# Kernel optimization log

Hardware: AMD Instinct MI355X
Metric: run time of the kernel (lower is better)

Reference implementation:

```python
import jax, jax.numpy as jnp
import numpy as np

N = 50000      # nodes
E = 800000     # edges (avg degree 16)
C_IN = 128
C_HID = 256
C_OUT = 256
SLOPE = 0.2    # LeakyReLU negative slope (PyG GATv2Conv default)


def gatv2_layer(x, src, dst, edge_attr, Wl, Wr, We, att, bias):
    """PyG GATv2Conv, heads=1, share_weights=False.
    e_ij = att . leaky_relu(Wl x_j + Wr x_i + We e_ij); softmax over incoming
    edges of each target i; out_i = sum_j alpha_ij * (Wl x_j) + bias."""
    xl = x @ Wl                       # [N, out] source transform
    xr = x @ Wr                       # [N, out] target transform
    ee = edge_attr[:, None] @ We      # [E, out] edge feature transform (edge_dim=1)
    m = xl[src] + xr[dst] + ee        # [E, out] per-edge message pre-activation
    e = jnp.einsum('ed,d->e', jax.nn.leaky_relu(m, SLOPE), att)  # [E]
    # segment softmax over target nodes
    emax = jax.ops.segment_max(e, dst, num_segments=N)           # [N]
    ex = jnp.exp(e - emax[dst])                                  # [E]
    denom = jax.ops.segment_sum(ex, dst, num_segments=N)         # [N]
    alpha = ex / denom[dst]                                      # [E]
    out = jax.ops.segment_sum(xl[src] * alpha[:, None], dst, num_segments=N)
    return out + bias


def setup_inputs() -> dict:
    key = jax.random.key(0)
    ks = jax.random.split(key, 24)

    def lin(k, i, o):
        return (jax.random.normal(k, (i, o), jnp.float32) / np.sqrt(i)).astype(jnp.float32)

    inp = {
        'features': jax.random.normal(ks[0], (N, C_IN), jnp.float32),
        'edge_index': jax.random.randint(ks[1], (2, E), 0, N, dtype=jnp.int64),
        'edge_attr': jax.random.uniform(ks[2], (E,), jnp.float32),
        # conv1: c_in -> c_hidden
        'Wl1': lin(ks[3], C_IN, C_HID), 'Wr1': lin(ks[4], C_IN, C_HID),
        'We1': lin(ks[5], 1, C_HID),
        'a1': jax.random.normal(ks[6], (C_HID,), jnp.float32) / np.sqrt(C_HID),
        'bb1': jnp.zeros((C_HID,), jnp.float32),
        # conv2: c_hidden -> c_hidden
        'Wl2': lin(ks[7], C_HID, C_HID), 'Wr2': lin(ks[8], C_HID, C_HID),
        'We2': lin(ks[9], 1, C_HID),
        'a2': jax.random.normal(ks[10], (C_HID,), jnp.float32) / np.sqrt(C_HID),
        'bb2': jnp.zeros((C_HID,), jnp.float32),
        # conv3: c_hidden -> c_out (concat=False, heads=1 -> same math)
        'Wl3': lin(ks[11], C_HID, C_OUT), 'Wr3': lin(ks[12], C_HID, C_OUT),
        'We3': lin(ks[13], 1, C_OUT),
        'a3': jax.random.normal(ks[14], (C_OUT,), jnp.float32) / np.sqrt(C_OUT),
        'bb3': jnp.zeros((C_OUT,), jnp.float32),
        # MLP head: Linear(c_out,10) -> relu -> Linear(10,1); dropout is eval-mode identity
        'Wh1': lin(ks[15], C_OUT, 10), 'bh1': jnp.zeros((10,), jnp.float32),
        'Wh2': lin(ks[16], 10, 1), 'bh2': jnp.zeros((1,), jnp.float32),
    }
    return inp


def reference(features, edge_index, edge_attr,
              Wl1, Wr1, We1, a1, bb1,
              Wl2, Wr2, We2, a2, bb2,
              Wl3, Wr3, We3, a3, bb3,
              Wh1, bh1, Wh2, bh2):
    src, dst = edge_index[0], edge_index[1]
    x1 = jax.nn.relu(gatv2_layer(features, src, dst, edge_attr, Wl1, Wr1, We1, a1, bb1))
    x2 = jax.nn.relu(gatv2_layer(x1, src, dst, edge_attr, Wl2, Wr2, We2, a2, bb2))
    x3 = jax.nn.relu(gatv2_layer(x2, src, dst, edge_attr, Wl3, Wr3, We3, a3, bb3))
    x4 = jnp.max(x3, axis=-2)                 # global max pool over nodes -> [c_out]
    x5 = jax.nn.relu(x4 @ Wh1 + bh1)          # [10]
    return x5 @ Wh2 + bh2                     # [1]
```

## Files before the change

### kernel.cpp

```cpp
#include <hip/hip_runtime.h>
#include <cstddef>
#include <cstdint>

typedef __attribute__((ext_vector_type(8))) short short8v;
typedef __attribute__((ext_vector_type(4))) short short4v;
typedef __attribute__((ext_vector_type(4))) float floatx4;

__device__ __forceinline__ float b2f(short u){
    return __uint_as_float(((unsigned)(unsigned short)u) << 16);
}
__device__ __forceinline__ short f2b(float f){
    unsigned x = __float_as_uint(f);
    unsigned r = x + 0x7FFFu + ((x >> 16) & 1u);
    return (short)(r >> 16);
}
__device__ __forceinline__ float loadF(const void* p, size_t i, int isBf16){
    return isBf16 ? b2f(((const short*)p)[i]) : ((const float*)p)[i];
}
__device__ __forceinline__ int loadI(const void* p, size_t i, int isI64){
    return isI64 ? ((const int*)p)[2 * i] : ((const int*)p)[i];
}
__device__ __forceinline__ void gload16(const void* g, void* l){
    __builtin_amdgcn_global_load_lds(
        (const __attribute__((address_space(1))) void*)g,
        (__attribute__((address_space(3))) void*)l, 16, 0, 0);
}

__global__ void setup_kernel(const void* feat, const void* ei, int N, int* flags,
                             int* cnt, int* fill, unsigned* pool, void* out){
    int gid = blockIdx.x * 256 + threadIdx.x;
    if (gid < N){ cnt[gid] = 0; fill[gid] = 0; }
    if (gid < 256) pool[gid] = 0u;
    if (blockIdx.x == 0){
        int t = threadIdx.x;
        if (t < 64){
            if (t >= 8 && t < 16) flags[t] = 0;
            const unsigned short* fs = (const unsigned short*)feat;
            int plaus = 0;
            for (int j = t; j < 128; j += 64){
                unsigned short s = fs[2 * j];
                int e = (s >> 7) & 0xFF;
                if (s == 0 || (e >= 100 && e <= 140)) plaus++;
            }
            #pragma unroll
            for (int o = 32; o > 0; o >>= 1) plaus += __shfl_xor(plaus, o);
            const int* ew = (const int*)ei;
            int zeros = 0;
            for (int j = t; j < 128; j += 64) if (ew[2 * j + 1] == 0) zeros++;
            #pragma unroll
            for (int o = 32; o > 0; o >>= 1) zeros += __shfl_xor(zeros, o);
            if (t == 0){
                flags[0] = (plaus >= 64) ? 1 : 0;
                flags[1] = (zeros >= 64) ? 1 : 0;
            }
        }
        __syncthreads();
        if (threadIdx.x == 0){
            if (flags[0]) ((short*)out)[0] = f2b(777.0f);
            else          ((float*)out)[0] = 777.0f;
        }
    }
}

__global__ void sentinel_kernel(void* out, const int* flags, float v){
    if (threadIdx.x == 0){
        if (flags[0]) ((short*)out)[0] = f2b(v);
        else          ((float*)out)[0] = v;
    }
}

__global__ void hist_kernel(const void* __restrict__ ei, int* __restrict__ cnt, int E,
                            const int* __restrict__ flags){
    int i = blockIdx.x * 256 + threadIdx.x;
    if (i < E) atomicAdd(&cnt[loadI(ei, (size_t)E + i, flags[1])], 1);
}

__global__ void scanA(const int* __restrict__ cnt, int* __restrict__ off,
                      int* __restrict__ partial, int N){
    __shared__ int wsum[16];
    const int t = threadIdx.x, w = t >> 6, lane = t & 63;
    int i = blockIdx.x * 1024 + t;
    int v = (i < N) ? cnt[i] : 0;
    int x = v;
    #pragma unroll
    for (int o = 1; o < 64; o <<= 1){
        int y = __shfl_up(x, o);
        if (lane >= o) x += y;
    }
    if (lane == 63) wsum[w] = x;
    __syncthreads();
    if (w == 0){
        int mv = (lane < 16) ? wsum[lane] : 0;
        int xx = mv;
        #pragma unroll
        for (int o = 1; o < 16; o <<= 1){
            int y = __shfl_up(xx, o);
            if (lane >= o) xx += y;
        }
        if (lane < 16) wsum[lane] = xx - mv;
    }
    __syncthreads();
    int incl = x + wsum[w];
    if (i < N) off[i] = incl - v;
    if (t == 1023) partial[blockIdx.x] = incl;
}

__global__ void scanB(int* __restrict__ partial, int* __restrict__ off, int nb, int N){
    int lane = threadIdx.x;
    int v = (lane < nb) ? partial[lane] : 0;
    int x = v;
    #pragma unroll
    for (int o = 1; o < 64; o <<= 1){
        int y = __shfl_up(x, o);
        if (lane >= o) x += y;
    }
    if (lane < nb) partial[lane] = x - v;
    if (lane == 63) off[N] = x;
}

__global__ void scanC(int* __restrict__ off, const int* __restrict__ partial, int N){
    int i = blockIdx.x * 1024 + threadIdx.x;
    if (i < N) off[i] += partial[blockIdx.x];
}

__global__ void scatter_kernel(const void* __restrict__ ei, const void* __restrict__ ea,
                               const int* __restrict__ off, int* __restrict__ fill,
                               int* __restrict__ srcS, float* __restrict__ eaS,
                               int E, const int* __restrict__ flags){
    int i = blockIdx.x * 256 + threadIdx.x;
    if (i >= E) return;
    int d = loadI(ei, (size_t)E + i, flags[1]);
    int pos = off[d] + atomicAdd(&fill[d], 1);
    srcS[pos] = loadI(ei, (size_t)i, flags[1]);
    eaS[pos] = loadF(ea, (size_t)i, flags[0]);
}

struct PJobs { const void* W[6]; short* bhi[6]; short* blo[6]; int K[6]; int fidx[6]; };
__global__ void prep_all(PJobs J, int* __restrict__ flags){
    int j = blockIdx.y;
    int K = J.K[j];
    if (blockIdx.x >= K) return;
    int idx = blockIdx.x * 256 + threadIdx.x;
    int k = idx >> 8, c = idx & 255;
    float v = loadF(J.W[j], idx, flags[0]);
    short h = f2b(v);
    short l = f2b(v - b2f(h));
    J.bhi[j][(size_t)c * K + k] = h;
    J.blo[j][(size_t)c * K + k] = l;
    if (__ballot(l != 0) != 0ull && (threadIdx.x & 63) == 0) atomicOr(&flags[J.fidx[j]], 1);
}

struct DJob { const void* src; float* dst; int n; };
struct DJobs { DJob j[13]; };
__global__ void decode_many(DJobs jobs, const int* __restrict__ flags){
    const DJob J = jobs.j[blockIdx.x];
    int fbf = flags[0];
    for (int i = threadIdx.x; i < J.n; i += 256)
        J.dst[i] = loadF(J.src, (size_t)i, fbf);
}

template<int BZ>
__global__ __launch_bounds__(512, 2) void gemm_tpl(
        const void* __restrict__ A, const short* __restrict__ Alo, int aRaw,
        const short* __restrict__ Bhi, const short* __restrict__ Blo,
        float* __restrict__ C, int M, int K,
        const int* __restrict__ flags, const int* __restrict__ bLoFlag){
    if (BZ ? (bLoFlag[0] != 0) : (bLoFlag[0] == 0)) return;
    __shared__ __align__(16) short Ah[2][256 * 32];
    __shared__ __align__(16) short Al[2][256 * 32];
    __shared__ __align__(16) short Bh[2][64 * 32];
    __shared__ __align__(16) short Bl[2][BZ ? 8 : 64 * 32];
    const int fbf = flags[0];
    const int az   = (aRaw && fbf) ? 1 : 0;
    const int aF32 = (aRaw && !fbf) ? 1 : 0;
    const int t = threadIdx.x;
    const int w = t >> 6, lane = t & 63;
    const int wrow = w >> 1, wcol = w & 1;
    const int bRow = blockIdx.x * 256;
    const int bCol = blockIdx.y * 64;
    const short* Ahp = (const short*)A;
    const float* Af  = (const float*)A;

    floatx4 acc[4][2];
    #pragma unroll
    for (int m = 0; m < 4; m++)
        #pragma unroll
        for (int n = 0; n < 2; n++) acc[m][n] = (floatx4){0.f, 0.f, 0.f, 0.f};

    auto STAGE = [&](int buf, int kk){
        if (!aF32){
            #pragma unroll
            for (int iss = 0; iss < 2; iss++){
                int ci  = (iss * 8 + w) * 64 + lane;
                int row = ci >> 2;
                int cg  = (ci & 3) ^ (row & 3);
                int gr = bRow + row; if (gr >= M) gr = M - 1;
                size_t ga = (size_t)gr * K + kk + cg * 8;
                int seg = (iss * 8 + w) * 512;
                gload16(&Ahp[ga], &Ah[buf][seg]);
                if (!az) gload16(&Alo[ga], &Al[buf][seg]);
            }
        } else {
            #pragma unroll
            for (int i2 = 0; i2 < 2; i2++){
                int e = i2 * 512 + t;
                int row = e >> 2, cl = e & 3;
                int slot = cl ^ (row & 3);
                int gr = bRow + row; if (gr >= M) gr = M - 1;
                size_t ga = (size_t)gr * K + kk + cl * 8;
                floatx4 v0 = *(const floatx4*)&Af[ga];
                floatx4 v1 = *(const floatx4*)&Af[ga + 4];
                short8v h, l;
                #pragma unroll
                for (int j = 0; j < 4; j++){
                    short hj = f2b(v0[j]);
                    h[j] = hj; l[j] = f2b(v0[j] - b2f(hj));
                    short hk = f2b(v1[j]);
                    h[4 + j] = hk; l[4 + j] = f2b(v1[j] - b2f(hk));
                }
                *(short8v*)&Ah[buf][row * 32 + slot * 8] = h;
                *(short8v*)&Al[buf][row * 32 + slot * 8] = l;
            }
        }
        {
            int ci  = w * 32 + (lane & 31);
            int row = ci >> 2;
            int cg  = (ci & 3) ^ (row & 3);
            size_t gb = (size_t)(bCol + row) * K + kk + cg * 8;
            int seg = w * 256;
            if (lane < 32){
                gload16(&Bhi[gb], &Bh[buf][seg]);
                if (!BZ) gload16(&Blo[gb], &Bl[buf][seg]);
            }
        }
    };

    const int T = K >> 5;
    STAGE(0, 0);
    int cur = 0;
    for (int kt = 0; kt < T; ++kt){
        if (kt + 1 < T) STAGE(cur ^ 1, (kt + 1) << 5);
        if (aF32){
            asm volatile("s_waitcnt vmcnt(0) lgkmcnt(0)" ::: "memory");
        } else if (kt + 1 >= T){
            asm volatile("s_waitcnt vmcnt(0)" ::: "memory");
        } else if (az){
            if (BZ) asm volatile("s_waitcnt vmcnt(3)" ::: "memory");
            else    asm volatile("s_waitcnt vmcnt(4)" ::: "memory");
        } else {
            if (BZ) asm volatile("s_waitcnt vmcnt(5)" ::: "memory");
            else    asm volatile("s_waitcnt vmcnt(6)" ::: "memory");
        }
        __builtin_amdgcn_s_barrier();
        const int g = lane >> 4;
        short8v a_h[4], a_l[4], b_h[2], b_l[2];
        #pragma unroll
        for (int m = 0; m < 4; m++){
            int ar = wrow * 64 + m * 16 + (lane & 15);
            int co = ((g ^ (ar & 3)) << 3);
            a_h[m] = *(const short8v*)&Ah[cur][ar * 32 + co];
            if (!az) a_l[m] = *(const short8v*)&Al[cur][ar * 32 + co];
        }
        #pragma unroll
        for (int n = 0; n < 2; n++){
            int br = wcol * 32 + n * 16 + (lane & 15);
            int co = ((g ^ (br & 3)) << 3);
            b_h[n] = *(const short8v*)&Bh[cur][br * 32 + co];
            if (!BZ) b_l[n] = *(const short8v*)&Bl[cur][br * 32 + co];
        }
        #pragma unroll
        for (int m = 0; m < 4; m++)
            #pragma unroll
            for (int n = 0; n < 2; n++){
                if (!az) acc[m][n] = __builtin_amdgcn_mfma_f32_16x16x32_bf16(
                                         a_l[m], b_h[n], acc[m][n], 0, 0, 0);
                if (!BZ) acc[m][n] = __builtin_amdgcn_mfma_f32_16x16x32_bf16(
                                         a_h[m], b_l[n], acc[m][n], 0, 0, 0);
                acc[m][n] = __builtin_amdgcn_mfma_f32_16x16x32_bf16(
                                a_h[m], b_h[n], acc[m][n], 0, 0, 0);
            }
        __builtin_amdgcn_s_barrier();
        cur ^= 1;
    }
    #pragma unroll
    for (int m = 0; m < 4; m++){
        int rb = bRow + wrow * 64 + m * 16 + ((lane >> 4) << 2);
        #pragma unroll
        for (int n = 0; n < 2; n++){
            int cg = bCol + wcol * 32 + n * 16 + (lane & 15);
            #pragma unroll
            for (int r = 0; r < 4; r++){
                int gr = rb + r;
                if (gr < M) C[(size_t)gr * 512 + cg] = acc[m][n][r];
            }
        }
    }
}

__global__ __launch_bounds__(256) void fused_agg(const float* __restrict__ PR,
        const int* __restrict__ srcS, const float* __restrict__ eaS,
        const int* __restrict__ off, const float* __restrict__ WeF,
        const float* __restrict__ attF, const float* __restrict__ bbF,
        short* __restrict__ QHi, short* __restrict__ QLo, int N){
    int node = blockIdx.x * 4 + (threadIdx.x >> 6);
    int lane = threadIdx.x & 63;
    if (node >= N) return;
    const int beg = off[node], end = off[node + 1];
    const int dd = lane << 2;
    const floatx4 xr4 = *(const floatx4*)&PR[(size_t)node * 512 + 256 + dd];
    const floatx4 we4 = *(const floatx4*)&WeF[dd];
    const floatx4 at4 = *(const floatx4*)&attF[dd];
    float m = -1e30f, ssum = 0.f;
    floatx4 a4 = (floatx4){0.f, 0.f, 0.f, 0.f};
    for (int k0 = beg; k0 < end; k0 += 8){
        floatx4 v[8]; float pp[8]; float eav[8];
        #pragma unroll
        for (int c = 0; c < 8; c++){
            int k = k0 + c; if (k >= end) k = end - 1;
            int s = srcS[k];
            eav[c] = eaS[k];
            v[c] = *(const floatx4*)&PR[(size_t)s * 512 + dd];
        }
        #pragma unroll
        for (int c = 0; c < 8; c++){
            float p = 0.f;
            #pragma unroll
            for (int j = 0; j < 4; j++){
                float tv = v[c][j] + xr4[j] + eav[c] * we4[j];
                tv = tv > 0.f ? tv : 0.2f * tv;
                p += tv * at4[j];
            }
            #pragma unroll
            for (int o = 32; o > 0; o >>= 1) p += __shfl_xor(p, o);
            pp[c] = (k0 + c < end) ? p : -1e30f;
        }
        float pm = pp[0];
        #pragma unroll
        for (int c = 1; c < 8; c++) pm = fmaxf(pm, pp[c]);
        float newm = fmaxf(m, pm);
        float scale = __expf(m - newm);
        ssum *= scale;
        a4[0] *= scale; a4[1] *= scale; a4[2] *= scale; a4[3] *= scale;
        #pragma unroll
        for (int c = 0; c < 8; c++){
            float wgt = __expf(pp[c] - newm);
            ssum += wgt;
            a4[0] += wgt * v[c][0]; a4[1] += wgt * v[c][1];
            a4[2] += wgt * v[c][2]; a4[3] += wgt * v[c][3];
        }
        m = newm;
    }
    float inv = (end > beg) ? 1.f / ssum : 0.f;
    short4v h4, l4;
    #pragma unroll
    for (int j = 0; j < 4; j++){
        float o = fmaxf(a4[j] * inv + bbF[dd + j], 0.f);
        short h = f2b(o);
        h4[j] = h;
        l4[j] = f2b(o - b2f(h));
    }
    *(short4v*)&QHi[(size_t)node * 256 + dd] = h4;
    *(short4v*)&QLo[(size_t)node * 256 + dd] = l4;
}

__global__ __launch_bounds__(256) void col_max2(const short* __restrict__ hi,
        const short* __restrict__ lo, unsigned* __restrict__ pool, int N){
    int lane = threadIdx.x & 63;
    int w = threadIdx.x >> 6;
    int dd = lane << 2;
    floatx4 mx = (floatx4){0.f, 0.f, 0.f, 0.f};
    for (int r = blockIdx.x * 4 + w; r < N; r += gridDim.x * 4){
        short4v h = *(const short4v*)&hi[(size_t)r * 256 + dd];
        short4v l = *(const short4v*)&lo[(size_t)r * 256 + dd];
        mx[0] = fmaxf(mx[0], b2f(h[0]) + b2f(l[0]));
        mx[1] = fmaxf(mx[1], b2f(h[1]) + b2f(l[1]));
        mx[2] = fmaxf(mx[2], b2f(h[2]) + b2f(l[2]));
        mx[3] = fmaxf(mx[3], b2f(h[3]) + b2f(l[3]));
    }
    atomicMax(&pool[dd + 0], __float_as_uint(mx[0]));
    atomicMax(&pool[dd + 1], __float_as_uint(mx[1]));
    atomicMax(&pool[dd + 2], __float_as_uint(mx[2]));
    atomicMax(&pool[dd + 3], __float_as_uint(mx[3]));
}

__global__ void head_kernel(const unsigned* __restrict__ pool, const float* __restrict__ Wh1F,
        const float* __restrict__ bh1F, const float* __restrict__ Wh2F,
        const float* __restrict__ bh2F, void* __restrict__ out, const int* __restrict__ flags){
    int lane = threadIdx.x;
    float acc = 0.f;
    if (lane < 10){
        acc = bh1F[lane];
        for (int d = 0; d < 256; ++d)
            acc += __uint_as_float(pool[d]) * Wh1F[d * 10 + lane];
        acc = fmaxf(acc, 0.f) * Wh2F[lane];
    }
    #pragma unroll
    for (int o = 32; o > 0; o >>= 1) acc += __shfl_xor(acc, o);
    if (lane == 0){
        float r = acc + bh2F[0];
        if (flags[0]) ((short*)out)[0] = f2b(r);
        else          ((float*)out)[0] = r;
    }
}

extern "C" void kernel_launch(void* const* d_in, const int* in_sizes, int n_in,
                              void* d_out, int out_size, void* d_ws, size_t ws_size,
                              hipStream_t stream){
    const void* feat = d_in[0];
    const void* ei   = d_in[1];
    const void* ea   = d_in[2];
    const void* Wl[3] = {d_in[3], d_in[8],  d_in[13]};
    const void* Wr[3] = {d_in[4], d_in[9],  d_in[14]};
    const void* We[3] = {d_in[5], d_in[10], d_in[15]};
    const void* at[3] = {d_in[6], d_in[11], d_in[16]};
    const void* bb[3] = {d_in[7], d_in[12], d_in[17]};
    const void* Wh1 = d_in[18];
    const void* bh1 = d_in[19];
    const void* Wh2 = d_in[20];
    const void* bh2 = d_in[21];

    const int N = in_sizes[0] / 128;
    const int E = in_sizes[1] / 2;
    const int Kin[3] = {128, 256, 256};
    const int nb = (N + 1023) / 1024;

    char* p = (char*)d_ws;
    auto alloc = [&](size_t bytes) -> void* {
        void* r = (void*)p; p += (bytes + 255) & ~(size_t)255; return r;
    };
    int*   flags   = (int*)alloc(256);
    int*   partial = (int*)alloc(256 * 4);
    int*   off   = (int*)alloc((size_t)(N + 1) * 4);
    int*   cnt   = (int*)alloc((size_t)N * 4);
    int*   fill  = (int*)alloc((size_t)N * 4);
    int*   srcS  = (int*)alloc((size_t)E * 4);
    float* eaS   = (float*)alloc((size_t)E * 4);
    float* PR    = (float*)alloc((size_t)N * 512 * 4);
    short* QHi   = (short*)alloc((size_t)N * 256 * 2);
    short* QLo   = (short*)alloc((size_t)N * 256 * 2);
    short* BtH[3]; short* BtL[3];
    for (int i = 0; i < 3; i++){
        BtH[i] = (short*)alloc((size_t)512 * Kin[i] * 2);
        BtL[i] = (short*)alloc((size_t)512 * Kin[i] * 2);
    }
    float* WeF  = (float*)alloc(3 * 256 * 4);
    float* attF = (float*)alloc(3 * 256 * 4);
    float* bbF  = (float*)alloc(3 * 256 * 4);
    float* Wh1F = (float*)alloc(2560 * 4);
    float* bh1F = (float*)alloc(16 * 4);
    float* Wh2F = (float*)alloc(16 * 4);
    float* bh2F = (float*)alloc(4 * 4);
    unsigned* pool = (unsigned*)alloc(256 * 4);
    size_t need = (size_t)(p - (char*)d_ws);

    setup_kernel<<<dim3((N + 255) / 256), dim3(256), 0, stream>>>(feat, ei, N, flags,
                                                                  cnt, fill, pool, d_out);
    if (need > ws_size){
        sentinel_kernel<<<dim3(1), dim3(1), 0, stream>>>(d_out, flags, 555.0f);
        return;
    }

    hist_kernel<<<dim3((E + 255) / 256), dim3(256), 0, stream>>>(ei, cnt, E, flags);
    scanA<<<dim3(nb), dim3(1024), 0, stream>>>(cnt, off, partial, N);
    scanB<<<dim3(1), dim3(64), 0, stream>>>(partial, off, nb, N);
    scanC<<<dim3(nb), dim3(1024), 0, stream>>>(off, partial, N);
    scatter_kernel<<<dim3((E + 255) / 256), dim3(256), 0, stream>>>(ei, ea, off, fill,
                                                                    srcS, eaS, E, flags);
    PJobs pj;
    for (int i = 0; i < 3; i++){
        pj.W[2 * i]     = Wl[i];
        pj.bhi[2 * i]   = BtH[i];
        pj.blo[2 * i]   = BtL[i];
        pj.W[2 * i + 1]   = Wr[i];
        pj.bhi[2 * i + 1] = BtH[i] + (size_t)256 * Kin[i];
        pj.blo[2 * i + 1] = BtL[i] + (size_t)256 * Kin[i];
        pj.K[2 * i] = pj.K[2 * i + 1] = Kin[i];
        pj.fidx[2 * i] = pj.fidx[2 * i + 1] = 8 + i;
    }
    prep_all<<<dim3(256, 6), dim3(256), 0, stream>>>(pj, flags);

    DJobs jobs;
    for (int i = 0; i < 3; i++){
        jobs.j[i]     = { We[i], WeF  + i * 256, 256 };
        jobs.j[3 + i] = { at[i], attF + i * 256, 256 };
        jobs.j[6 + i] = { bb[i], bbF  + i * 256, 256 };
    }
    jobs.j[9]  = { Wh1, Wh1F, 2560 };
    jobs.j[10] = { bh1, bh1F, 10 };
    jobs.j[11] = { Wh2, Wh2F, 10 };
    jobs.j[12] = { bh2, bh2F, 1 };
    decode_many<<<dim3(13), dim3(256), 0, stream>>>(jobs, flags);

    dim3 gemm_grid((N + 255) / 256, 8);
    for (int L = 0; L < 3; L++){
        const void* A = (L == 0) ? feat : (const void*)QHi;
        int aRaw = (L == 0) ? 1 : 0;
        gemm_tpl<1><<<gemm_grid, dim3(512), 0, stream>>>(A, QLo, aRaw, BtH[L], BtL[L],
                                                         PR, N, Kin[L], flags, &flags[8 + L]);
        gemm_tpl<0><<<gemm_grid, dim3(512), 0, stream>>>(A, QLo, aRaw, BtH[L], BtL[L],
                                                         PR, N, Kin[L], flags, &flags[8 + L]);
        fused_agg<<<dim3((N + 3) / 4), dim3(256), 0, stream>>>(PR, srcS, eaS, off,
                                                               WeF + L * 256, attF + L * 256,
                                                               bbF + L * 256, QHi, QLo, N);
    }
    col_max2<<<dim3(256), dim3(256), 0, stream>>>(QHi, QLo, pool, N);
    head_kernel<<<dim3(1), dim3(64), 0, stream>>>(pool, Wh1F, bh1F, Wh2F, bh2F, d_out, flags);
    (void)n_in; (void)out_size;
}
```

Before: 892.4 us.

## Retile GEMM to 128x128 blocks, specialize A-zero path, use DPP wave reduction

The split-bf16 GEMM moves from 256x64 tiles with 512 threads to 128x128 tiles with 256 threads, each wave now computing a 64x64 sub-tile, and B staging is merged into the same load loop. A new template variant skips the A-low products and their loads entirely when the raw input is already bf16. This aims for better operand reuse per tile and higher occupancy. The aggregation kernel's shuffle-xor reduction is replaced by a DPP row-shift reduction with a final readlane, and it gets an occupancy hint. The trade-off is more accumulator registers per thread and more kernel launches in the first layer.

```diff
diff --git a/kernel.cpp b/kernel.cpp
--- a/kernel.cpp
+++ b/kernel.cpp
@@ -24,6 +24,21 @@
     __builtin_amdgcn_global_load_lds(
         (const __attribute__((address_space(1))) void*)g,
         (__attribute__((address_space(3))) void*)l, 16, 0, 0);
+}
+
+template<int CTRL, int RM>
+__device__ __forceinline__ float dppAdd(float p){
+    int t = __builtin_amdgcn_update_dpp(0, __float_as_int(p), CTRL, RM, 0xF, true);
+    return p + __int_as_float(t);
+}
+__device__ __forceinline__ float waveSum(float p){
+    p = dppAdd<0xB1, 0xF>(p);
+    p = dppAdd<0x4E, 0xF>(p);
+    p = dppAdd<0x141, 0xF>(p);
+    p = dppAdd<0x140, 0xF>(p);
+    p = dppAdd<0x142, 0xA>(p);
+    p = dppAdd<0x143, 0xC>(p);
+    return __int_as_float(__builtin_amdgcn_readlane(__float_as_int(p), 63));
 }
 
 __global__ void setup_kernel(const void* feat, const void* ei, int N, int* flags,
@@ -159,52 +174,60 @@
         J.dst[i] = loadF(J.src, (size_t)i, fbf);
 }
 
-template<int BZ>
-__global__ __launch_bounds__(512, 2) void gemm_tpl(
+template<int AZT, int BZ>
+__global__ __launch_bounds__(256, (AZT && BZ) ? 4 : 3) void gemm_tpl(
         const void* __restrict__ A, const short* __restrict__ Alo, int aRaw,
         const short* __restrict__ Bhi, const short* __restrict__ Blo,
         float* __restrict__ C, int M, int K,
         const int* __restrict__ flags, const int* __restrict__ bLoFlag){
-    if (BZ ? (bLoFlag[0] != 0) : (bLoFlag[0] == 0)) return;
-    __shared__ __align__(16) short Ah[2][256 * 32];
-    __shared__ __align__(16) short Al[2][256 * 32];
-    __shared__ __align__(16) short Bh[2][64 * 32];
-    __shared__ __align__(16) short Bl[2][BZ ? 8 : 64 * 32];
     const int fbf = flags[0];
-    const int az   = (aRaw && fbf) ? 1 : 0;
-    const int aF32 = (aRaw && !fbf) ? 1 : 0;
+    const int azr = (aRaw && fbf) ? 1 : 0;
+    const int bLo = bLoFlag[0];
+    if (AZT){ if (!azr || bLo) return; }
+    else if (BZ){ if (azr || bLo) return; }
+    else { if (!bLo) return; }
+    __shared__ __align__(16) short Ah[2][128 * 32];
+    __shared__ __align__(16) short Al[2][AZT ? 8 : 128 * 32];
+    __shared__ __align__(16) short Bh[2][128 * 32];
+    __shared__ __align__(16) short Bl[2][BZ ? 8 : 128 * 32];
+    const int az   = AZT ? 1 : (BZ ? 0 : azr);
+    const int aF32 = AZT ? 0 : ((aRaw && !fbf) ? 1 : 0);
     const int t = threadIdx.x;
     const int w = t >> 6, lane = t & 63;
-    const int wrow = w >> 1, wcol = w & 1;
-    const int bRow = blockIdx.x * 256;
-    const int bCol = blockIdx.y * 64;
+    const int wr = w >> 1, wc = w & 1;
+    const int bRow = blockIdx.x * 128;
+    const int bCol = blockIdx.y * 128;
     const short* Ahp = (const short*)A;
     const float* Af  = (const float*)A;
 
-    floatx4 acc[4][2];
+    floatx4 acc[4][4];
     #pragma unroll
     for (int m = 0; m < 4; m++)
         #pragma unroll
-        for (int n = 0; n < 2; n++) acc[m][n] = (floatx4){0.f, 0.f, 0.f, 0.f};
+        for (int n = 0; n < 4; n++) acc[m][n] = (floatx4){0.f, 0.f, 0.f, 0.f};
 
     auto STAGE = [&](int buf, int kk){
-        if (!aF32){
+        #pragma unroll
+        for (int iss = 0; iss < 2; iss++){
+            int ci  = (iss * 4 + w) * 64 + lane;
+            int row = ci >> 2;
+            int cg  = (ci & 3) ^ (row & 3);
+            int gr = bRow + row; if (gr >= M) gr = M - 1;
+            size_t ga  = (size_t)gr * K + kk + cg * 8;
+            size_t gbi = (size_t)(bCol + row) * K + kk + cg * 8;
+            int seg = (iss * 4 + w) * 512;
+            if (!aF32){
+                gload16(&Ahp[ga], &Ah[buf][seg]);
+                if (!az) gload16(&Alo[ga], &Al[buf][seg]);
+            }
+            gload16(&Bhi[gbi], &Bh[buf][seg]);
+            if (!BZ) gload16(&Blo[gbi], &Bl[buf][seg]);
+        }
+        if (aF32){
             #pragma unroll
             for (int iss = 0; iss < 2; iss++){
-                int ci  = (iss * 8 + w) * 64 + lane;
-                int row = ci >> 2;
-                int cg  = (ci & 3) ^ (row & 3);
-                int gr = bRow + row; if (gr >= M) gr = M - 1;
-                size_t ga = (size_t)gr * K + kk + cg * 8;
-                int seg = (iss * 8 + w) * 512;
-                gload16(&Ahp[ga], &Ah[buf][seg]);
-                if (!az) gload16(&Alo[ga], &Al[buf][seg]);
-            }
-        } else {
-            #pragma unroll
-            for (int i2 = 0; i2 < 2; i2++){
-                int e = i2 * 512 + t;
-                int row = e >> 2, cl = e & 3;
+                int ci  = (iss * 4 + w) * 64 + lane;
+                int row = ci >> 2, cl = ci & 3;
                 int slot = cl ^ (row & 3);
                 int gr = bRow + row; if (gr >= M) gr = M - 1;
                 size_t ga = (size_t)gr * K + kk + cl * 8;
@@ -222,17 +245,6 @@
                 *(short8v*)&Al[buf][row * 32 + slot * 8] = l;
             }
         }
-        {
-            int ci  = w * 32 + (lane & 31);
-            int row = ci >> 2;
-            int cg  = (ci & 3) ^ (row & 3);
-            size_t gb = (size_t)(bCol + row) * K + kk + cg * 8;
-            int seg = w * 256;
-            if (lane < 32){
-                gload16(&Bhi[gb], &Bh[buf][seg]);
-                if (!BZ) gload16(&Blo[gb], &Bl[buf][seg]);
-            }
-        }
     };
 
     const int T = K >> 5;
@@ -245,33 +257,32 @@
         } else if (kt + 1 >= T){
             asm volatile("s_waitcnt vmcnt(0)" ::: "memory");
         } else if (az){
-            if (BZ) asm volatile("s_waitcnt vmcnt(3)" ::: "memory");
-            else    asm volatile("s_waitcnt vmcnt(4)" ::: "memory");
+            if (BZ) asm volatile("s_waitcnt vmcnt(4)" ::: "memory");
+            else    asm volatile("s_waitcnt vmcnt(6)" ::: "memory");
         } else {
-            if (BZ) asm volatile("s_waitcnt vmcnt(5)" ::: "memory");
-            else    asm volatile("s_waitcnt vmcnt(6)" ::: "memory");
+            if (BZ) asm volatile("s_waitcnt vmcnt(6)" ::: "memory");
+            else    asm volatile("s_waitcnt vmcnt(8)" ::: "memory");
         }
         __builtin_amdgcn_s_barrier();
-        const int g = lane >> 4;
-        short8v a_h[4], a_l[4], b_h[2], b_l[2];
+        short8v a_h[4], a_l[4], b_h[4], b_l[4];
         #pragma unroll
         for (int m = 0; m < 4; m++){
-            int ar = wrow * 64 + m * 16 + (lane & 15);
-            int co = ((g ^ (ar & 3)) << 3);
+            int ar = wr * 64 + m * 16 + (lane & 15);
+            int co = (((lane >> 4) ^ (ar & 3)) << 3);
             a_h[m] = *(const short8v*)&Ah[cur][ar * 32 + co];
             if (!az) a_l[m] = *(const short8v*)&Al[cur][ar * 32 + co];
         }
         #pragma unroll
-        for (int n = 0; n < 2; n++){
-            int br = wcol * 32 + n * 16 + (lane & 15);
-            int co = ((g ^ (br & 3)) << 3);
+        for (int n = 0; n < 4; n++){
+            int br = wc * 64 + n * 16 + (lane & 15);
+            int co = (((lane >> 4) ^ (br & 3)) << 3);
             b_h[n] = *(const short8v*)&Bh[cur][br * 32 + co];
             if (!BZ) b_l[n] = *(const short8v*)&Bl[cur][br * 32 + co];
         }
         #pragma unroll
         for (int m = 0; m < 4; m++)
             #pragma unroll
-            for (int n = 0; n < 2; n++){
+            for (int n = 0; n < 4; n++){
                 if (!az) acc[m][n] = __builtin_amdgcn_mfma_f32_16x16x32_bf16(
                                          a_l[m], b_h[n], acc[m][n], 0, 0, 0);
                 if (!BZ) acc[m][n] = __builtin_amdgcn_mfma_f32_16x16x32_bf16(
@@ -284,10 +295,10 @@
     }
     #pragma unroll
     for (int m = 0; m < 4; m++){
-        int rb = bRow + wrow * 64 + m * 16 + ((lane >> 4) << 2);
-        #pragma unroll
-        for (int n = 0; n < 2; n++){
-            int cg = bCol + wcol * 32 + n * 16 + (lane & 15);
+        int rb = bRow + wr * 64 + m * 16 + ((lane >> 4) << 2);
+        #pragma unroll
+        for (int n = 0; n < 4; n++){
+            int cg = bCol + wc * 64 + n * 16 + (lane & 15);
             #pragma unroll
             for (int r = 0; r < 4; r++){
                 int gr = rb + r;
@@ -297,7 +308,7 @@
     }
 }
 
-__global__ __launch_bounds__(256) void fused_agg(const float* __restrict__ PR,
+__global__ __launch_bounds__(256, 8) void fused_agg(const float* __restrict__ PR,
         const int* __restrict__ srcS, const float* __restrict__ eaS,
         const int* __restrict__ off, const float* __restrict__ WeF,
         const float* __restrict__ attF, const float* __restrict__ bbF,
@@ -330,9 +341,8 @@
                 tv = tv > 0.f ? tv : 0.2f * tv;
                 p += tv * at4[j];
             }
-            #pragma unroll
-            for (int o = 32; o > 0; o >>= 1) p += __shfl_xor(p, o);
-            pp[c] = (k0 + c < end) ? p : -1e30f;
+            float ps = waveSum(p);
+            pp[c] = (k0 + c < end) ? ps : -1e30f;
         }
         float pm = pp[0];
         #pragma unroll
@@ -491,14 +501,21 @@
     jobs.j[12] = { bh2, bh2F, 1 };
     decode_many<<<dim3(13), dim3(256), 0, stream>>>(jobs, flags);
 
-    dim3 gemm_grid((N + 255) / 256, 8);
+    dim3 gemm_grid((N + 127) / 128, 4);
     for (int L = 0; L < 3; L++){
         const void* A = (L == 0) ? feat : (const void*)QHi;
         int aRaw = (L == 0) ? 1 : 0;
-        gemm_tpl<1><<<gemm_grid, dim3(512), 0, stream>>>(A, QLo, aRaw, BtH[L], BtL[L],
-                                                         PR, N, Kin[L], flags, &flags[8 + L]);
-        gemm_tpl<0><<<gemm_grid, dim3(512), 0, stream>>>(A, QLo, aRaw, BtH[L], BtL[L],
-                                                         PR, N, Kin[L], flags, &flags[8 + L]);
+        if (L == 0){
+            gemm_tpl<1,1><<<gemm_grid, dim3(256), 0, stream>>>(A, QLo, aRaw, BtH[L], BtL[L],
+                                                               PR, N, Kin[L], flags, &flags[8 + L]);
+            gemm_tpl<0,1><<<gemm_grid, dim3(256), 0, stream>>>(A, QLo, aRaw, BtH[L], BtL[L],
+                                                               PR, N, Kin[L], flags, &flags[8 + L]);
+        } else {
+            gemm_tpl<0,1><<<gemm_grid, dim3(256), 0, stream>>>(A, QLo, aRaw, BtH[L], BtL[L],
+                                                               PR, N, Kin[L], flags, &flags[8 + L]);
+        }
+        gemm_tpl<0,0><<<gemm_grid, dim3(256), 0, stream>>>(A, QLo, aRaw, BtH[L], BtL[L],
+                                                           PR, N, Kin[L], flags, &flags[8 + L]);
         fused_agg<<<dim3((N + 3) / 4), dim3(256), 0, stream>>>(PR, srcS, eaS, off,
                                                                WeF + L * 256, attF + L * 256,
                                                                bbF + L * 256, QHi, QLo, N);
```

Measured after the change: 1.869 ms. 109% more time.
